# Optimization experiments

Hardware: AMD Instinct MI355X
Metric: run time of the kernel (lower is better)

Reference implementation:

```python
import jax, jax.numpy as jnp
import numpy as np

H, W = 256, 256
FX, FY = 300.0, 300.0
CX, CY = 128.0, 128.0
N = 1024
B = 2
EPS = 1e-8


def setup_inputs() -> dict:
    key = jax.random.key(0)
    ks = jax.random.split(key, 6)
    positions = jax.random.normal(ks[0], (N, 3), jnp.float32)
    # keep points in front of the camera (positive depth)
    positions = positions.at[:, 2].set(jnp.abs(positions[:, 2]) + 3.0)
    colors = jax.random.uniform(ks[1], (N, 3), jnp.float32)
    opacities = jax.random.uniform(ks[2], (N, 1), jnp.float32)
    # gaussian footprint of 5..20 pixels (scales are in pixel units)
    scales = 5.0 + 15.0 * jax.random.uniform(ks[3], (N, 1), jnp.float32)
    qvec = jax.random.normal(ks[4], (B, 4), jnp.float32)
    tvec = 0.1 * jax.random.normal(ks[5], (B, 3), jnp.float32)
    xs = jnp.arange(W, dtype=jnp.float32)
    ys = jnp.arange(H, dtype=jnp.float32)
    yy, xx = jnp.meshgrid(ys, xs, indexing='ij')
    pixel_coords = jnp.stack([xx.reshape(-1), yy.reshape(-1)], axis=1)  # [HW,2]
    return dict(positions=positions, colors=colors, opacities=opacities,
                scales=scales, qvec=qvec, tvec=tvec, pixel_coords=pixel_coords)


def _quat_to_rot(q):
    q = q / jnp.linalg.norm(q)
    w, x, y, z = q[0], q[1], q[2], q[3]
    return jnp.stack([
        jnp.stack([1 - 2 * (y * y + z * z), 2 * (x * y - z * w), 2 * (x * z + y * w)]),
        jnp.stack([2 * (x * y + z * w), 1 - 2 * (x * x + z * z), 2 * (y * z - x * w)]),
        jnp.stack([2 * (x * z - y * w), 2 * (y * z + x * w), 1 - 2 * (x * x + y * y)]),
    ])


def reference(positions, colors, opacities, scales, qvec, tvec, pixel_coords):
    # [N,1] per-gaussian isotropic variance (pixel^2)
    var = scales[:, :1] ** 2
    c2 = (pixel_coords ** 2).sum(-1)  # [HW]

    def render_one(q, t):
        R = _quat_to_rot(q)
        p_cam = positions @ R.T + t  # [N,3]
        xy = p_cam[:, :2] / p_cam[:, 2:3]
        proj = xy * jnp.array([FX, FY], jnp.float32) + jnp.array([CX, CY], jnp.float32)  # [N,2]
        # ||c - p||^2 expansion avoids the [N,HW,2] diff tensor of the original
        dist2 = (proj ** 2).sum(-1)[:, None] + c2[None, :] - 2.0 * (proj @ pixel_coords.T)  # [N,HW]
        w = opacities * jnp.exp(-0.5 * dist2 / var)  # [N,HW]
        num = w.T @ colors                 # [HW,3]
        den = w.sum(0)[:, None] + EPS      # [HW,1]
        return (num / den).T.reshape(3, H, W)

    return jax.vmap(render_one)(qvec, tvec)  # [B,3,H,W]
```

## Files before the change

### kernel.cpp

```cpp
#include <hip/hip_runtime.h>
#include <cmath>

#define HH 256
#define WW 256
#define NG 1024
#define NB 2
#define NTILE 256
static constexpr float FXc = 300.0f;
static constexpr float FYc = 300.0f;
static constexpr float CXc = 128.0f;
static constexpr float CYc = 128.0f;
static constexpr float EPSc = 1e-8f;
static constexpr float LOG2E = 1.4426950408889634f;

#if defined(__has_builtin)
#if __has_builtin(__builtin_amdgcn_exp2f)
#define FAST_EXP2(x) __builtin_amdgcn_exp2f(x)
#else
#define FAST_EXP2(x) exp2f(x)
#endif
#else
#define FAST_EXP2(x) exp2f(x)
#endif

__global__ __launch_bounds__(512) void render_kernel(
    const float* __restrict__ positions,
    const float* __restrict__ colors,
    const float* __restrict__ opacities,
    const float* __restrict__ scales,
    const float* __restrict__ qvec,
    const float* __restrict__ tvec,
    float* __restrict__ out)
{
    __shared__ float4 gs0[NG];
    __shared__ float4 gs1[NG];
    __shared__ int wcnt[8];

    const int b = blockIdx.x >> 8;
    int tile = blockIdx.x & 255;
    if (b) tile ^= 128;
    const int x0 = (tile & 7) << 5;
    const int y0 = (tile >> 3) << 3;
    const float cx = (float)x0 + 15.5f;
    const float cy = (float)y0 + 3.5f;

    float qw = qvec[b * 4 + 0], qx = qvec[b * 4 + 1];
    float qy = qvec[b * 4 + 2], qz = qvec[b * 4 + 3];
    float rin = rsqrtf(qw * qw + qx * qx + qy * qy + qz * qz);
    qw *= rin; qx *= rin; qy *= rin; qz *= rin;
    const float r00 = 1.0f - 2.0f * (qy * qy + qz * qz);
    const float r01 = 2.0f * (qx * qy - qz * qw);
    const float r02 = 2.0f * (qx * qz + qy * qw);
    const float r10 = 2.0f * (qx * qy + qz * qw);
    const float r11 = 1.0f - 2.0f * (qx * qx + qz * qz);
    const float r12 = 2.0f * (qy * qz - qx * qw);
    const float r20 = 2.0f * (qx * qz - qy * qw);
    const float r21 = 2.0f * (qy * qz + qx * qw);
    const float r22 = 1.0f - 2.0f * (qx * qx + qy * qy);
    const float t0 = tvec[b * 3 + 0], t1 = tvec[b * 3 + 1], t2 = tvec[b * 3 + 2];

    const int wv = threadIdx.x >> 6;
    const int lane = threadIdx.x & 63;

    float4 pa0, pa1, pc0, pc1;
    int pos0 = -1, pos1 = -1;
    int cnt = 0;

    #pragma unroll
    for (int r = 0; r < 2; ++r) {
        const int g = wv * 128 + r * 64 + lane;
        const float X = positions[g * 3 + 0];
        const float Y = positions[g * 3 + 1];
        const float Z = positions[g * 3 + 2];
        const float cxp = r00 * X + r01 * Y + r02 * Z + t0;
        const float cyp = r10 * X + r11 * Y + r12 * Z + t1;
        const float czp = r20 * X + r21 * Y + r22 * Z + t2;
        const float iz = 1.0f / czp;
        const float ux = cxp * iz * FXc + CXc;
        const float uy = cyp * iz * FYc + CYc;
        const float s = scales[g];
        const float rcut = 7.8987f * s;
        const float ddx = fmaxf(fabsf(ux - cx) - 15.5f, 0.0f);
        const float ddy = fmaxf(fabsf(uy - cy) - 3.5f, 0.0f);
        const bool in = fmaf(ddx, ddx, ddy * ddy) <= rcut * rcut;
        const unsigned long long m = __ballot(in);
        if (in) {
            const float k = -0.5f * LOG2E / (s * s);
            const float lop = __log2f(opacities[g]);
            const float kx = -2.0f * k * ux;
            const float ky = -2.0f * k * uy;
            const float A = fmaf(k, fmaf(ux, ux, uy * uy), lop);
            const int pre = cnt + __popcll(m & ((1ull << lane) - 1ull));
            if (r == 0) {
                pa0 = make_float4(k, kx, ky, A);
                pc0 = make_float4(colors[g * 3 + 0], colors[g * 3 + 1],
                                  colors[g * 3 + 2], 0.0f);
                pos0 = pre;
            } else {
                pa1 = make_float4(k, kx, ky, A);
                pc1 = make_float4(colors[g * 3 + 0], colors[g * 3 + 1],
                                  colors[g * 3 + 2], 0.0f);
                pos1 = pre;
            }
        }
        cnt += __popcll(m);
    }
    if (lane == 0) wcnt[wv] = cnt;
    __syncthreads();

    int base = 0, npTot = 0;
    #pragma unroll
    for (int j = 0; j < 8; ++j) {
        const int c = wcnt[j];
        if (j < wv) base += c;
        npTot += c;
    }
    if (pos0 >= 0) { gs0[base + pos0] = pa0; gs1[base + pos0] = pc0; }
    if (pos1 >= 0) { gs0[base + pos1] = pa1; gs1[base + pos1] = pc1; }
    const int np = (npTot + 7) & ~7;
    if ((int)threadIdx.x < np - npTot) {
        gs0[npTot + threadIdx.x] = make_float4(0.0f, 0.0f, 0.0f, -500.0f);
        gs1[npTot + threadIdx.x] = make_float4(0.0f, 0.0f, 0.0f, 0.0f);
    }
    __syncthreads();

    const int h = threadIdx.x & 7;
    const int t = threadIdx.x >> 3;
    const int px0i = x0 + ((t & 15) << 1);
    const int py0i = y0 + ((t >> 4) << 1);
    const float px = (float)px0i;
    const float py = (float)py0i;
    const float c2 = fmaf(px, px, py * py);
    const float u = fmaf(2.0f, px, 1.0f);
    const float v = fmaf(2.0f, py, 1.0f);

    float4 aden = make_float4(0.f, 0.f, 0.f, 0.f);
    float4 ar = aden, ag = aden, ab = aden;

    const int iters = np >> 3;
    #pragma unroll 4
    for (int i = 0; i < iters; ++i) {
        const int g = (i << 3) + h;
        const float4 g0 = gs0[g];
        const float4 g1 = gs1[g];
        const float k = g0.x;
        float e00 = fmaf(k, c2, g0.w);
        e00 = fmaf(g0.y, px, e00);
        e00 = fmaf(g0.z, py, e00);
        const float d10 = fminf(fmaf(k, u, g0.y), 126.0f);
        const float d01 = fminf(fmaf(k, v, g0.z), 126.0f);
        const float w00 = FAST_EXP2(e00);
        const float Ex = FAST_EXP2(d10);
        const float Ey = FAST_EXP2(d01);
        const float w10 = w00 * Ex;
        const float w01 = w00 * Ey;
        const float w11 = w10 * Ey;
        aden.x += w00; aden.y += w10; aden.z += w01; aden.w += w11;
        ar.x = fmaf(w00, g1.x, ar.x); ar.y = fmaf(w10, g1.x, ar.y);
        ar.z = fmaf(w01, g1.x, ar.z); ar.w = fmaf(w11, g1.x, ar.w);
        ag.x = fmaf(w00, g1.y, ag.x); ag.y = fmaf(w10, g1.y, ag.y);
        ag.z = fmaf(w01, g1.y, ag.z); ag.w = fmaf(w11, g1.y, ag.w);
        ab.x = fmaf(w00, g1.z, ab.x); ab.y = fmaf(w10, g1.z, ab.y);
        ab.z = fmaf(w01, g1.z, ab.z); ab.w = fmaf(w11, g1.z, ab.w);
    }

    #pragma unroll
    for (int m = 1; m <= 4; m <<= 1) {
        aden.x += __shfl_xor(aden.x, m); aden.y += __shfl_xor(aden.y, m);
        aden.z += __shfl_xor(aden.z, m); aden.w += __shfl_xor(aden.w, m);
        ar.x += __shfl_xor(ar.x, m); ar.y += __shfl_xor(ar.y, m);
        ar.z += __shfl_xor(ar.z, m); ar.w += __shfl_xor(ar.w, m);
        ag.x += __shfl_xor(ag.x, m); ag.y += __shfl_xor(ag.y, m);
        ag.z += __shfl_xor(ag.z, m); ag.w += __shfl_xor(ag.w, m);
        ab.x += __shfl_xor(ab.x, m); ab.y += __shfl_xor(ab.y, m);
        ab.z += __shfl_xor(ab.z, m); ab.w += __shfl_xor(ab.w, m);
    }

    if (h < 4) {
        float den, cr, cg, cb;
        if (h == 0)      { den = aden.x; cr = ar.x; cg = ag.x; cb = ab.x; }
        else if (h == 1) { den = aden.y; cr = ar.y; cg = ag.y; cb = ab.y; }
        else if (h == 2) { den = aden.z; cr = ar.z; cg = ag.z; cb = ab.z; }
        else             { den = aden.w; cr = ar.w; cg = ag.w; cb = ab.w; }
        const int pxx = px0i + (h & 1);
        const int pyy = py0i + (h >> 1);
        const float inv = 1.0f / (den + EPSc);
        const size_t o = (size_t)b * 3 * 65536 + (size_t)pyy * WW + pxx;
        out[o]           = cr * inv;
        out[o + 65536]   = cg * inv;
        out[o + 131072]  = cb * inv;
    }
}

extern "C" void kernel_launch(void* const* d_in, const int* in_sizes, int n_in,
                              void* d_out, int out_size, void* d_ws, size_t ws_size,
                              hipStream_t stream) {
    const float* positions = (const float*)d_in[0];
    const float* colors    = (const float*)d_in[1];
    const float* opacities = (const float*)d_in[2];
    const float* scales    = (const float*)d_in[3];
    const float* qvec      = (const float*)d_in[4];
    const float* tvec      = (const float*)d_in[5];
    float* out = (float*)d_out;

    render_kernel<<<dim3(NB * NTILE), dim3(512), 0, stream>>>(
        positions, colors, opacities, scales, qvec, tvec, out);
}
```

Measured before the change: 12.24 us.

## Compute 4x2 pixel octets per thread with packed FP32 accumulation

Each thread now covers a 4x2 pixel block instead of a 2x2 quad, with 16 threads splitting the gaussian list instead of 8. A second exp2 plus a precomputed per-gaussian factor G4 (stored in the spare color slot) produces the shifted columns, and all accumulators are float2 vectors so the compiler can emit packed FMA and packed add instructions. The aim is fewer exp evaluations and FMA instructions per pixel. In exchange it uses more registers and a longer shuffle reduction, and pads the gaussian list to a multiple of 16.

New measurement: 14.48 us. +18.3%, slower.

```diff
diff --git a/kernel.cpp b/kernel.cpp
--- a/kernel.cpp
+++ b/kernel.cpp
@@ -23,6 +23,14 @@
 #define FAST_EXP2(x) exp2f(x)
 #endif
 
+typedef __attribute__((ext_vector_type(2))) float f32x2;
+static __device__ __forceinline__ f32x2 splat2(float s) {
+    f32x2 v; v.x = s; v.y = s; return v;
+}
+static __device__ __forceinline__ f32x2 pkshfl_xor(f32x2 v, int m) {
+    f32x2 r; r.x = __shfl_xor(v.x, m); r.y = __shfl_xor(v.y, m); return r;
+}
+
 __global__ __launch_bounds__(512) void render_kernel(
     const float* __restrict__ positions,
     const float* __restrict__ colors,
@@ -33,7 +41,7 @@
     float* __restrict__ out)
 {
     __shared__ float4 gs0[NG];
-    __shared__ float4 gs1[NG];
+    __shared__ float4 gsC[NG];
     __shared__ int wcnt[8];
 
     const int b = blockIdx.x >> 8;
@@ -90,16 +98,17 @@
             const float kx = -2.0f * k * ux;
             const float ky = -2.0f * k * uy;
             const float A = fmaf(k, fmaf(ux, ux, uy * uy), lop);
+            const float G4 = exp2f(4.0f * k);
             const int pre = cnt + __popcll(m & ((1ull << lane) - 1ull));
             if (r == 0) {
                 pa0 = make_float4(k, kx, ky, A);
                 pc0 = make_float4(colors[g * 3 + 0], colors[g * 3 + 1],
-                                  colors[g * 3 + 2], 0.0f);
+                                  colors[g * 3 + 2], G4);
                 pos0 = pre;
             } else {
                 pa1 = make_float4(k, kx, ky, A);
                 pc1 = make_float4(colors[g * 3 + 0], colors[g * 3 + 1],
-                                  colors[g * 3 + 2], 0.0f);
+                                  colors[g * 3 + 2], G4);
                 pos1 = pre;
             }
         }
@@ -115,76 +124,105 @@
         if (j < wv) base += c;
         npTot += c;
     }
-    if (pos0 >= 0) { gs0[base + pos0] = pa0; gs1[base + pos0] = pc0; }
-    if (pos1 >= 0) { gs0[base + pos1] = pa1; gs1[base + pos1] = pc1; }
-    const int np = (npTot + 7) & ~7;
+    if (pos0 >= 0) { gs0[base + pos0] = pa0; gsC[base + pos0] = pc0; }
+    if (pos1 >= 0) { gs0[base + pos1] = pa1; gsC[base + pos1] = pc1; }
+    const int np = (npTot + 15) & ~15;
     if ((int)threadIdx.x < np - npTot) {
         gs0[npTot + threadIdx.x] = make_float4(0.0f, 0.0f, 0.0f, -500.0f);
-        gs1[npTot + threadIdx.x] = make_float4(0.0f, 0.0f, 0.0f, 0.0f);
+        gsC[npTot + threadIdx.x] = make_float4(0.0f, 0.0f, 0.0f, 1.0f);
     }
     __syncthreads();
 
-    const int h = threadIdx.x & 7;
-    const int t = threadIdx.x >> 3;
-    const int px0i = x0 + ((t & 15) << 1);
-    const int py0i = y0 + ((t >> 4) << 1);
-    const float px = (float)px0i;
-    const float py = (float)py0i;
+    const int h = threadIdx.x & 15;
+    const int t = threadIdx.x >> 4;
+    const int octx = x0 + ((t & 7) << 2);
+    const int octy = y0 + ((t >> 3) << 1);
+    const float px = (float)octx;
+    const float py = (float)octy;
     const float c2 = fmaf(px, px, py * py);
     const float u = fmaf(2.0f, px, 1.0f);
     const float v = fmaf(2.0f, py, 1.0f);
 
-    float4 aden = make_float4(0.f, 0.f, 0.f, 0.f);
-    float4 ar = aden, ag = aden, ab = aden;
-
-    const int iters = np >> 3;
-    #pragma unroll 4
+    f32x2 zz = {0.f, 0.f};
+    f32x2 d0A = zz, d0B = zz, r0A = zz, r0B = zz;
+    f32x2 g0A = zz, g0B = zz, b0A = zz, b0B = zz;
+    f32x2 d1A = zz, d1B = zz, r1A = zz, r1B = zz;
+    f32x2 g1A = zz, g1B = zz, b1A = zz, b1B = zz;
+
+    const int iters = np >> 4;
+    #pragma unroll 2
     for (int i = 0; i < iters; ++i) {
-        const int g = (i << 3) + h;
-        const float4 g0 = gs0[g];
-        const float4 g1 = gs1[g];
-        const float k = g0.x;
-        float e00 = fmaf(k, c2, g0.w);
-        e00 = fmaf(g0.y, px, e00);
-        e00 = fmaf(g0.z, py, e00);
-        const float d10 = fminf(fmaf(k, u, g0.y), 126.0f);
-        const float d01 = fminf(fmaf(k, v, g0.z), 126.0f);
+        const int g = (i << 4) + h;
+        const float4 q0 = gs0[g];
+        const float4 qc = gsC[g];
+        const float k = q0.x;
+        float e00 = fmaf(k, c2, q0.w);
+        e00 = fmaf(q0.y, px, e00);
+        e00 = fmaf(q0.z, py, e00);
+        const float d10u = fmaf(k, u, q0.y);
+        const float d01u = fmaf(k, v, q0.z);
+        const float e02 = fmaf(2.0f, d10u + k, e00);
+        const float d10 = fminf(d10u, 126.0f);
+        const float d01 = fminf(d01u, 126.0f);
         const float w00 = FAST_EXP2(e00);
-        const float Ex = FAST_EXP2(d10);
-        const float Ey = FAST_EXP2(d01);
+        const float Ex  = FAST_EXP2(d10);
+        const float Ey  = FAST_EXP2(d01);
+        const float w02 = FAST_EXP2(e02);
+        const float ExB = Ex * qc.w;
         const float w10 = w00 * Ex;
-        const float w01 = w00 * Ey;
-        const float w11 = w10 * Ey;
-        aden.x += w00; aden.y += w10; aden.z += w01; aden.w += w11;
-        ar.x = fmaf(w00, g1.x, ar.x); ar.y = fmaf(w10, g1.x, ar.y);
-        ar.z = fmaf(w01, g1.x, ar.z); ar.w = fmaf(w11, g1.x, ar.w);
-        ag.x = fmaf(w00, g1.y, ag.x); ag.y = fmaf(w10, g1.y, ag.y);
-        ag.z = fmaf(w01, g1.y, ag.z); ag.w = fmaf(w11, g1.y, ag.w);
-        ab.x = fmaf(w00, g1.z, ab.x); ab.y = fmaf(w10, g1.z, ab.y);
-        ab.z = fmaf(w01, g1.z, ab.z); ab.w = fmaf(w11, g1.z, ab.w);
+        const float w12 = w02 * ExB;
+        f32x2 WA0; WA0.x = w00; WA0.y = w10;
+        f32x2 WA1; WA1.x = w02; WA1.y = w12;
+        const f32x2 ey2 = splat2(Ey);
+        const f32x2 WB0 = WA0 * ey2;
+        const f32x2 WB1 = WA1 * ey2;
+        const f32x2 rr = splat2(qc.x);
+        const f32x2 gg = splat2(qc.y);
+        const f32x2 bb = splat2(qc.z);
+        d0A += WA0; d0B += WB0; d1A += WA1; d1B += WB1;
+        r0A = __builtin_elementwise_fma(WA0, rr, r0A);
+        r0B = __builtin_elementwise_fma(WB0, rr, r0B);
+        r1A = __builtin_elementwise_fma(WA1, rr, r1A);
+        r1B = __builtin_elementwise_fma(WB1, rr, r1B);
+        g0A = __builtin_elementwise_fma(WA0, gg, g0A);
+        g0B = __builtin_elementwise_fma(WB0, gg, g0B);
+        g1A = __builtin_elementwise_fma(WA1, gg, g1A);
+        g1B = __builtin_elementwise_fma(WB1, gg, g1B);
+        b0A = __builtin_elementwise_fma(WA0, bb, b0A);
+        b0B = __builtin_elementwise_fma(WB0, bb, b0B);
+        b1A = __builtin_elementwise_fma(WA1, bb, b1A);
+        b1B = __builtin_elementwise_fma(WB1, bb, b1B);
     }
 
     #pragma unroll
-    for (int m = 1; m <= 4; m <<= 1) {
-        aden.x += __shfl_xor(aden.x, m); aden.y += __shfl_xor(aden.y, m);
-        aden.z += __shfl_xor(aden.z, m); aden.w += __shfl_xor(aden.w, m);
-        ar.x += __shfl_xor(ar.x, m); ar.y += __shfl_xor(ar.y, m);
-        ar.z += __shfl_xor(ar.z, m); ar.w += __shfl_xor(ar.w, m);
-        ag.x += __shfl_xor(ag.x, m); ag.y += __shfl_xor(ag.y, m);
-        ag.z += __shfl_xor(ag.z, m); ag.w += __shfl_xor(ag.w, m);
-        ab.x += __shfl_xor(ab.x, m); ab.y += __shfl_xor(ab.y, m);
-        ab.z += __shfl_xor(ab.z, m); ab.w += __shfl_xor(ab.w, m);
-    }
-
-    if (h < 4) {
-        float den, cr, cg, cb;
-        if (h == 0)      { den = aden.x; cr = ar.x; cg = ag.x; cb = ab.x; }
-        else if (h == 1) { den = aden.y; cr = ar.y; cg = ag.y; cb = ab.y; }
-        else if (h == 2) { den = aden.z; cr = ar.z; cg = ag.z; cb = ab.z; }
-        else             { den = aden.w; cr = ar.w; cg = ag.w; cb = ab.w; }
-        const int pxx = px0i + (h & 1);
-        const int pyy = py0i + (h >> 1);
+    for (int m = 1; m <= 8; m <<= 1) {
+        d0A += pkshfl_xor(d0A, m); d0B += pkshfl_xor(d0B, m);
+        d1A += pkshfl_xor(d1A, m); d1B += pkshfl_xor(d1B, m);
+        r0A += pkshfl_xor(r0A, m); r0B += pkshfl_xor(r0B, m);
+        r1A += pkshfl_xor(r1A, m); r1B += pkshfl_xor(r1B, m);
+        g0A += pkshfl_xor(g0A, m); g0B += pkshfl_xor(g0B, m);
+        g1A += pkshfl_xor(g1A, m); g1B += pkshfl_xor(g1B, m);
+        b0A += pkshfl_xor(b0A, m); b0B += pkshfl_xor(b0B, m);
+        b1A += pkshfl_xor(b1A, m); b1B += pkshfl_xor(b1B, m);
+    }
+
+    if (h < 8) {
+        const int xo = h & 3;
+        const int yo = h >> 2;
+        const bool q1 = xo >= 2;
+        const bool rowB = yo != 0;
+        const f32x2 dsel = q1 ? (rowB ? d1B : d1A) : (rowB ? d0B : d0A);
+        const f32x2 rsel = q1 ? (rowB ? r1B : r1A) : (rowB ? r0B : r0A);
+        const f32x2 gsel = q1 ? (rowB ? g1B : g1A) : (rowB ? g0B : g0A);
+        const f32x2 bsel = q1 ? (rowB ? b1B : b1A) : (rowB ? b0B : b0A);
+        const bool odd = (xo & 1) != 0;
+        const float den = odd ? dsel.y : dsel.x;
+        const float cr  = odd ? rsel.y : rsel.x;
+        const float cg  = odd ? gsel.y : gsel.x;
+        const float cb  = odd ? bsel.y : bsel.x;
         const float inv = 1.0f / (den + EPSc);
+        const int pxx = octx + xo;
+        const int pyy = octy + yo;
         const size_t o = (size_t)b * 3 * 65536 + (size_t)pyy * WW + pxx;
         out[o]           = cr * inv;
         out[o + 65536]   = cg * inv;
```
